# Performance work log

Hardware: AMD Instinct MI355X
Metric: run time of the kernel (lower is better)

## Reference

```python
import jax, jax.numpy as jnp
import numpy as np

# Dims from init_kwargs / input_specs
C_IN, H, W = 128, 224, 224
C_OUT, KH, KW = 256, 3, 3
STRIDE = 1  # padding='valid'


def setup_inputs() -> dict:
    key = jax.random.key(0)
    k1, k2 = jax.random.split(key)
    x = jax.random.normal(k1, (C_IN, H, W), dtype=jnp.float32)
    kernels = jax.random.normal(k2, (C_OUT, C_IN, KH, KW), dtype=jnp.float32) * 0.05
    return {"x": x, "kernels": kernels}


def reference(x, kernels):
    # Original does im2col + matmul, which is exactly a valid cross-correlation
    # (no kernel flip). Express it as a direct conv: (1,C,H,W) * (O,I,kh,kw).
    out = jax.lax.conv_general_dilated(
        x[None],                      # (1, C_in, H, W)
        kernels,                      # (C_out, C_in, KH, KW)
        window_strides=(STRIDE, STRIDE),
        padding="VALID",
        dimension_numbers=("NCHW", "OIHW", "NCHW"),
    )
    return out[0]                     # (C_out, H_out, W_out) = (256, 222, 222)
```

## Files before the change

### kernel.cpp

```cpp
#include <hip/hip_runtime.h>

#define CIN   128
#define HH    224
#define WW    224
#define COUT  256
#define HO    222
#define WO    222

typedef unsigned short u16;
typedef unsigned int   u32;
typedef __bf16  bf16x8 __attribute__((ext_vector_type(8)));
typedef float   f32x4  __attribute__((ext_vector_type(4)));

__device__ __forceinline__ u16 f2bf(float f) {
  union { float f; u32 u; } v; v.f = f;
  u32 u = v.u;
  return (u16)((u + 0x7FFFu + ((u >> 16) & 1u)) >> 16);
}

__global__ void prep(const float* __restrict__ x, const float* __restrict__ w,
                     u16* __restrict__ xp, u16* __restrict__ wp) {
  const int t = threadIdx.x;
  if (blockIdx.x < 448) {
    const int xcd = blockIdx.x & 7;
    const int q   = blockIdx.x >> 3;
    const int h   = xcd * 28 + (q >> 1);
    const int wb  = q & 1;
    __shared__ u16 tile[128][116];
#pragma unroll
    for (int i = 0; i < 14; ++i) {
      int idx = i * 256 + t;
      int c   = idx / 28;
      int wq  = idx % 28;
      float4 v = *(const float4*)(&x[(size_t)c * (HH * WW) + h * WW + wb * 112 + wq * 4]);
      uint2 p;
      p.x = (u32)f2bf(v.x) | ((u32)f2bf(v.y) << 16);
      p.y = (u32)f2bf(v.z) | ((u32)f2bf(v.w) << 16);
      *(uint2*)(&tile[c][wq * 4]) = p;
    }
    __syncthreads();
#pragma unroll
    for (int i = 0; i < 7; ++i) {
      int idx  = i * 256 + t;
      int wl   = idx >> 4;
      int jcp  = idx & 15;
      int ww   = wb * 112 + wl;
      int jsrc = jcp ^ (ww & 15);
      uint4 v;
      v.x = (u32)tile[jsrc * 8 + 0][wl] | ((u32)tile[jsrc * 8 + 1][wl] << 16);
      v.y = (u32)tile[jsrc * 8 + 2][wl] | ((u32)tile[jsrc * 8 + 3][wl] << 16);
      v.z = (u32)tile[jsrc * 8 + 4][wl] | ((u32)tile[jsrc * 8 + 5][wl] << 16);
      v.w = (u32)tile[jsrc * 8 + 6][wl] | ((u32)tile[jsrc * 8 + 7][wl] << 16);
      *(uint4*)(&xp[((size_t)h * WW + ww) * 128 + jcp * 8]) = v;
    }
  } else {
    int u    = (blockIdx.x - 448) * 256 + t;
    int jcp  = u & 7;
    int mr   = (u >> 3) & 127;
    int rest = u >> 10;
    int kw   = rest % 3;
    int q    = rest / 3;
    int ch   = q & 1;
    int r    = q >> 1;
    int kh   = r % 3;
    int mt   = r / 3;
    int oc   = mt * 128 + mr;
    int cb   = ch * 64 + (jcp ^ (mr & 7)) * 8;
    u16 o[8];
#pragma unroll
    for (int e = 0; e < 8; ++e)
      o[e] = f2bf(w[((size_t)(oc * CIN + cb + e) * 3 + kh) * 3 + kw]);
    uint4 v;
    v.x = (u32)o[0] | ((u32)o[1] << 16);
    v.y = (u32)o[2] | ((u32)o[3] << 16);
    v.z = (u32)o[4] | ((u32)o[5] << 16);
    v.w = (u32)o[6] | ((u32)o[7] << 16);
    *(uint4*)(&wp[(size_t)u * 8]) = v;
  }
}

__device__ __forceinline__ void lds_dma16(const u16* g, u16* l) {
  __builtin_amdgcn_global_load_lds(
      reinterpret_cast<__attribute__((address_space(1))) u32*>(
          reinterpret_cast<uintptr_t>(g)),
      reinterpret_cast<__attribute__((address_space(3))) u32*>(
          reinterpret_cast<uintptr_t>(l)),
      16, 0, 0);
}

__global__ __launch_bounds__(256, 2) void conv_mfma(const u16* __restrict__ wp,
                                                    const u16* __restrict__ xp,
                                                    float* __restrict__ out) {
  __shared__ u16 ldsB[226 * 128];

  const int tid  = threadIdx.x;
  const int lane = tid & 63;
  const int wave = tid >> 6;
  const int quad = lane >> 4;
  const int lr   = lane & 15;
  const int wm   = wave >> 1;
  const int wn   = wave & 1;

  const int bx  = blockIdx.x;
  const int xcd = bx & 7;
  const int mt  = (bx >> 3) & 1;
  const int oh  = xcd * 28 + (bx >> 4);
  if (oh >= HO) return;

  f32x4 acc[4][7];
#pragma unroll
  for (int i = 0; i < 4; ++i)
#pragma unroll
    for (int j = 0; j < 7; ++j) acc[i][j] = {0.f, 0.f, 0.f, 0.f};

  int swA[2];
#pragma unroll
  for (int k2 = 0; k2 < 2; ++k2)
    swA[k2] = ((k2 * 4 + quad) ^ (lr & 7)) << 3;

  for (int kh = 0; kh < 3; ++kh) {
    const u16* g = xp + (size_t)(oh + kh) * (WW * 128);

    __syncthreads();
#pragma unroll
    for (int uu = 0; uu < 14; ++uu) {
      const int unit = wave * 14 + uu;
      lds_dma16(g + unit * 512 + lane * 8, &ldsB[unit * 512]);
    }
    __syncthreads();

    const u16* Ab = wp + (size_t)(mt * 3 + kh) * 2 * 24576 + wm * 4096 + lr * 64;

#pragma unroll
    for (int kw = 0; kw < 3; ++kw) {
      bf16x8 af[4][4];
#pragma unroll
      for (int ks = 0; ks < 4; ++ks) {
        const u16* Ak = Ab + (ks >> 1) * 24576 + kw * 8192;
#pragma unroll
        for (int i = 0; i < 4; ++i)
          af[ks][i] = *reinterpret_cast<const bf16x8*>(Ak + i * 1024 + swA[ks & 1]);
      }

      const int bq   = (wn * 112 + lr + kw) * 128;
      const int sw15 = (lr + kw) & 15;
#pragma unroll
      for (int ks = 0; ks < 4; ++ks) {
        const int swB = ((ks * 4 + quad) ^ sw15) << 3;
        bf16x8 bg[7];
#pragma unroll
        for (int j = 0; j < 7; ++j)
          bg[j] = *reinterpret_cast<const bf16x8*>(&ldsB[bq + j * 2048 + swB]);
#pragma unroll
        for (int i = 0; i < 4; ++i)
#pragma unroll
          for (int j = 0; j < 7; ++j)
            acc[i][j] = __builtin_amdgcn_mfma_f32_16x16x32_bf16(af[ks][i], bg[j], acc[i][j], 0, 0, 0);
      }
    }
  }

  const int mb = mt * 128 + wm * 64;
#pragma unroll
  for (int i = 0; i < 4; ++i) {
#pragma unroll
    for (int j = 0; j < 7; ++j) {
      const int col = wn * 112 + j * 16 + lr;
      if (col < WO) {
        float* op = out + (size_t)(mb + i * 16 + quad * 4) * (HO * WO) +
                    (size_t)oh * WO + col;
#pragma unroll
        for (int r = 0; r < 4; ++r)
          op[(size_t)r * (HO * WO)] = acc[i][j][r];
      }
    }
  }
}

__global__ void conv_naive(const float* __restrict__ x, const float* __restrict__ w,
                           float* __restrict__ out) {
  int idx = blockIdx.x * 256 + threadIdx.x;
  if (idx >= COUT * HO * WO) return;
  int ow  = idx % WO;
  int tmp = idx / WO;
  int oh  = tmp % HO;
  int oc  = tmp / HO;
  float s = 0.f;
  for (int c = 0; c < CIN; ++c)
    for (int kh = 0; kh < 3; ++kh) {
      const float* xr = &x[(size_t)(c * HH + oh + kh) * WW + ow];
      const float* wr = &w[((size_t)(oc * CIN + c) * 3 + kh) * 3];
      s += xr[0] * wr[0] + xr[1] * wr[1] + xr[2] * wr[2];
    }
  out[idx] = s;
}

extern "C" void kernel_launch(void* const* d_in, const int* in_sizes, int n_in,
                              void* d_out, int out_size, void* d_ws, size_t ws_size,
                              hipStream_t stream) {
  const float* x    = (const float*)d_in[0];
  const float* kern = (const float*)d_in[1];
  float* out        = (float*)d_out;

  const size_t WP_BYTES = (size_t)36864 * 16;
  const size_t XP_BYTES = (size_t)HH * WW * 128 * 2;

  if (ws_size >= WP_BYTES + XP_BYTES) {
    u16* wp = (u16*)d_ws;
    u16* xp = (u16*)((char*)d_ws + WP_BYTES);
    hipLaunchKernelGGL(prep, dim3(592), dim3(256), 0, stream, x, kern, xp, wp);
    hipLaunchKernelGGL(conv_mfma, dim3(448), dim3(256), 0, stream, wp, xp, out);
  } else {
    int total = COUT * HO * WO;
    hipLaunchKernelGGL(conv_naive, dim3((total + 255) / 256), dim3(256), 0, stream,
                       x, kern, out);
  }
}
```

Measured before the change: 119.0 us.

## Drop LDS staging; load conv operands directly from global in single-wave blocks

Removes the shared-memory staging of the input row and the XOR swizzles in both the prep layout and the MFMA operand loads. Each 64-thread block now holds one wave's 64x112 output tile and reads A and B fragments straight from global memory (relying on L1/L2), with four times as many blocks. This drops the barriers and the LDS footprint, but each wave now re-fetches the shared input row from cache, which raises global and L2 traffic. The workspace-size threshold also gains an extra 1024 bytes.

```diff
diff --git a/kernel.cpp b/kernel.cpp
--- a/kernel.cpp
+++ b/kernel.cpp
@@ -43,19 +43,18 @@
     for (int i = 0; i < 7; ++i) {
       int idx  = i * 256 + t;
       int wl   = idx >> 4;
-      int jcp  = idx & 15;
+      int jc   = idx & 15;
       int ww   = wb * 112 + wl;
-      int jsrc = jcp ^ (ww & 15);
       uint4 v;
-      v.x = (u32)tile[jsrc * 8 + 0][wl] | ((u32)tile[jsrc * 8 + 1][wl] << 16);
-      v.y = (u32)tile[jsrc * 8 + 2][wl] | ((u32)tile[jsrc * 8 + 3][wl] << 16);
-      v.z = (u32)tile[jsrc * 8 + 4][wl] | ((u32)tile[jsrc * 8 + 5][wl] << 16);
-      v.w = (u32)tile[jsrc * 8 + 6][wl] | ((u32)tile[jsrc * 8 + 7][wl] << 16);
-      *(uint4*)(&xp[((size_t)h * WW + ww) * 128 + jcp * 8]) = v;
+      v.x = (u32)tile[jc * 8 + 0][wl] | ((u32)tile[jc * 8 + 1][wl] << 16);
+      v.y = (u32)tile[jc * 8 + 2][wl] | ((u32)tile[jc * 8 + 3][wl] << 16);
+      v.z = (u32)tile[jc * 8 + 4][wl] | ((u32)tile[jc * 8 + 5][wl] << 16);
+      v.w = (u32)tile[jc * 8 + 6][wl] | ((u32)tile[jc * 8 + 7][wl] << 16);
+      *(uint4*)(&xp[((size_t)h * WW + ww) * 128 + jc * 8]) = v;
     }
   } else {
     int u    = (blockIdx.x - 448) * 256 + t;
-    int jcp  = u & 7;
+    int jc   = u & 7;
     int mr   = (u >> 3) & 127;
     int rest = u >> 10;
     int kw   = rest % 3;
@@ -65,7 +64,7 @@
     int kh   = r % 3;
     int mt   = r / 3;
     int oc   = mt * 128 + mr;
-    int cb   = ch * 64 + (jcp ^ (mr & 7)) * 8;
+    int cb   = ch * 64 + jc * 8;
     u16 o[8];
 #pragma unroll
     for (int e = 0; e < 8; ++e)
@@ -79,33 +78,22 @@
   }
 }
 
-__device__ __forceinline__ void lds_dma16(const u16* g, u16* l) {
-  __builtin_amdgcn_global_load_lds(
-      reinterpret_cast<__attribute__((address_space(1))) u32*>(
-          reinterpret_cast<uintptr_t>(g)),
-      reinterpret_cast<__attribute__((address_space(3))) u32*>(
-          reinterpret_cast<uintptr_t>(l)),
-      16, 0, 0);
-}
-
-__global__ __launch_bounds__(256, 2) void conv_mfma(const u16* __restrict__ wp,
-                                                    const u16* __restrict__ xp,
-                                                    float* __restrict__ out) {
-  __shared__ u16 ldsB[226 * 128];
-
-  const int tid  = threadIdx.x;
-  const int lane = tid & 63;
-  const int wave = tid >> 6;
+__global__ __launch_bounds__(64, 2) void conv_mfma(const u16* __restrict__ wp,
+                                                   const u16* __restrict__ xp,
+                                                   float* __restrict__ out) {
+  const int lane = threadIdx.x;
   const int quad = lane >> 4;
   const int lr   = lane & 15;
-  const int wm   = wave >> 1;
-  const int wn   = wave & 1;
 
   const int bx  = blockIdx.x;
   const int xcd = bx & 7;
-  const int mt  = (bx >> 3) & 1;
-  const int oh  = xcd * 28 + (bx >> 4);
+  const int r   = bx >> 3;
+  const int oh  = xcd * 28 + (r >> 3);
   if (oh >= HO) return;
+  const int sub = r & 7;
+  const int mt  = sub & 1;
+  const int wm  = (sub >> 1) & 1;
+  const int wn  = sub >> 2;
 
   f32x4 acc[4][7];
 #pragma unroll
@@ -113,49 +101,28 @@
 #pragma unroll
     for (int j = 0; j < 7; ++j) acc[i][j] = {0.f, 0.f, 0.f, 0.f};
 
-  int swA[2];
-#pragma unroll
-  for (int k2 = 0; k2 < 2; ++k2)
-    swA[k2] = ((k2 * 4 + quad) ^ (lr & 7)) << 3;
-
   for (int kh = 0; kh < 3; ++kh) {
-    const u16* g = xp + (size_t)(oh + kh) * (WW * 128);
-
-    __syncthreads();
-#pragma unroll
-    for (int uu = 0; uu < 14; ++uu) {
-      const int unit = wave * 14 + uu;
-      lds_dma16(g + unit * 512 + lane * 8, &ldsB[unit * 512]);
-    }
-    __syncthreads();
-
-    const u16* Ab = wp + (size_t)(mt * 3 + kh) * 2 * 24576 + wm * 4096 + lr * 64;
+    const u16* Arow = wp + (size_t)(mt * 3 + kh) * 2 * 24576 + (wm * 64 + lr) * 64;
+    const u16* Brow = xp + (size_t)(oh + kh) * (WW * 128) + (wn * 112 + lr) * 128;
 
 #pragma unroll
     for (int kw = 0; kw < 3; ++kw) {
-      bf16x8 af[4][4];
 #pragma unroll
       for (int ks = 0; ks < 4; ++ks) {
-        const u16* Ak = Ab + (ks >> 1) * 24576 + kw * 8192;
+        const u16* Ak = Arow + (ks >> 1) * 24576 + kw * 8192 + ((ks & 1) * 4 + quad) * 8;
+        const u16* Bk = Brow + kw * 128 + (ks * 4 + quad) * 8;
+        bf16x8 af[4], bg[7];
 #pragma unroll
         for (int i = 0; i < 4; ++i)
-          af[ks][i] = *reinterpret_cast<const bf16x8*>(Ak + i * 1024 + swA[ks & 1]);
-      }
-
-      const int bq   = (wn * 112 + lr + kw) * 128;
-      const int sw15 = (lr + kw) & 15;
-#pragma unroll
-      for (int ks = 0; ks < 4; ++ks) {
-        const int swB = ((ks * 4 + quad) ^ sw15) << 3;
-        bf16x8 bg[7];
+          af[i] = *reinterpret_cast<const bf16x8*>(Ak + i * 1024);
 #pragma unroll
         for (int j = 0; j < 7; ++j)
-          bg[j] = *reinterpret_cast<const bf16x8*>(&ldsB[bq + j * 2048 + swB]);
+          bg[j] = *reinterpret_cast<const bf16x8*>(Bk + j * 2048);
 #pragma unroll
         for (int i = 0; i < 4; ++i)
 #pragma unroll
           for (int j = 0; j < 7; ++j)
-            acc[i][j] = __builtin_amdgcn_mfma_f32_16x16x32_bf16(af[ks][i], bg[j], acc[i][j], 0, 0, 0);
+            acc[i][j] = __builtin_amdgcn_mfma_f32_16x16x32_bf16(af[i], bg[j], acc[i][j], 0, 0, 0);
       }
     }
   }
@@ -170,8 +137,8 @@
         float* op = out + (size_t)(mb + i * 16 + quad * 4) * (HO * WO) +
                     (size_t)oh * WO + col;
 #pragma unroll
-        for (int r = 0; r < 4; ++r)
-          op[(size_t)r * (HO * WO)] = acc[i][j][r];
+        for (int r4 = 0; r4 < 4; ++r4)
+          op[(size_t)r4 * (HO * WO)] = acc[i][j][r4];
       }
     }
   }
@@ -205,11 +172,11 @@
   const size_t WP_BYTES = (size_t)36864 * 16;
   const size_t XP_BYTES = (size_t)HH * WW * 128 * 2;
 
-  if (ws_size >= WP_BYTES + XP_BYTES) {
+  if (ws_size >= WP_BYTES + XP_BYTES + 1024) {
     u16* wp = (u16*)d_ws;
     u16* xp = (u16*)((char*)d_ws + WP_BYTES);
     hipLaunchKernelGGL(prep, dim3(592), dim3(256), 0, stream, x, kern, xp, wp);
-    hipLaunchKernelGGL(conv_mfma, dim3(448), dim3(256), 0, stream, wp, xp, out);
+    hipLaunchKernelGGL(conv_mfma, dim3(1792), dim3(64), 0, stream, wp, xp, out);
   } else {
     int total = COUT * HO * WO;
     hipLaunchKernelGGL(conv_naive, dim3((total + 255) / 256), dim3(256), 0, stream,
```

Measured after the change: 170.3 us. +43.1%, slower.
